# Performance work log

Hardware: AMD Instinct MI355X
Metric: run time of the kernel (lower is better)

## Reference

```python
import jax, jax.numpy as jnp
import numpy as np

K_POS, K_NEG = 3, 2
MIN_D = 9  # min_dist=8 bumped to next odd, as in _nms_topk
BN_EPS = 1e-5


def _conv(x, w, pad):
    return jax.lax.conv_general_dilated(
        x, w, (1, 1), [(pad, pad), (pad, pad)],
        dimension_numbers=('NCHW', 'OIHW', 'NCHW'))


def _bn(x, g, b, m, v):
    scale = g * jax.lax.rsqrt(v + BN_EPS)  # inference-mode BN
    return x * scale[None, :, None, None] + (b - m * scale)[None, :, None, None]


def _head(x, w1, g1, b1, m1, v1, w2, g2, b2, m2, v2, w3, b3, out_hw):
    h = jax.nn.relu(_bn(_conv(x, w1, 1), g1, b1, m1, v1))
    h = jax.nn.relu(_bn(_conv(h, w2, 1), g2, b2, m2, v2))
    logits = _conv(h, w3, 0) + b3[None, :, None, None]
    B = logits.shape[0]
    # F.interpolate(mode='bilinear', align_corners=False) == half-pixel bilinear resize
    logits = jax.image.resize(logits, (B, 1, out_hw, out_hw), method='bilinear')
    return logits


def _sample_one(smap, key):
    # smap: [H, W] sigmoid heatmap for one sample
    H, W = smap.shape
    # --- positive points: NMS-style peak top-k ---
    local_max = jax.lax.reduce_window(
        smap, -jnp.inf, jax.lax.max, (MIN_D, MIN_D), (1, 1), 'SAME')
    is_peak = (smap == local_max) & (smap > 0.1)
    masked = jnp.where(is_peak, smap, -jnp.inf).reshape(-1)
    vals, idx = jax.lax.top_k(masked, K_POS)
    valid = jnp.isfinite(vals)  # slots corresponding to real peaks
    xs = jnp.where(valid, (idx % W).astype(jnp.float32), 0.0)
    ys = jnp.where(valid, (idx // W).astype(jnp.float32), 0.0)
    pos_lab = jnp.where(valid, 1, -1).astype(jnp.int32)
    # fallback: no peak at all -> single argmax point in slot 0
    amax = jnp.argmax(smap)
    any_peak = valid[0]
    xs = xs.at[0].set(jnp.where(any_peak, xs[0], (amax % W).astype(jnp.float32)))
    ys = ys.at[0].set(jnp.where(any_peak, ys[0], (amax // W).astype(jnp.float32)))
    pos_lab = pos_lab.at[0].set(1)  # slot 0 is always a positive point
    pos = jnp.stack([xs, ys], axis=1)  # [K_POS, 2] (x, y)
    # --- negative points: uniform sample from low-response region ---
    low = (smap < 0.3).reshape(-1)
    low_fb = (smap < smap.max()).reshape(-1)
    mask = jnp.where(jnp.any(low), low, low_fb)
    n = mask.sum()
    # stable argsort puts masked-in (True) flat indices first, in index order
    order = jnp.argsort(jnp.logical_not(mask))
    u = jax.random.uniform(key, (K_NEG,))
    ridx = jnp.minimum((u * jnp.maximum(n, 1).astype(jnp.float32)).astype(jnp.int32),
                       jnp.maximum(n - 1, 0))
    sel = order[ridx]
    neg = jnp.stack([sel % W, sel // W], axis=1).astype(jnp.float32)
    neg = jnp.where(n > 0, neg, jnp.zeros_like(neg))
    neg_lab = jnp.zeros((K_NEG,), jnp.int32)
    coords = jnp.concatenate([pos, neg], axis=0)      # [K_POS+K_NEG, 2]
    labels = jnp.concatenate([pos_lab, neg_lab], axis=0)
    return coords, labels


def setup_inputs() -> dict:
    key = jax.random.key(0)
    ks = jax.random.split(key, 4)
    B, C, h, w = 32, 256, 64, 64
    HID = 64
    x = jax.random.normal(ks[0], (B, C, h, w), jnp.float32)
    w1 = jax.random.normal(ks[1], (HID, C, 3, 3), jnp.float32) * 0.03  # kaiming-ish
    w2 = jax.random.normal(ks[2], (HID, HID, 3, 3), jnp.float32) * 0.06
    w3 = jax.random.normal(ks[3], (1, HID, 1, 1), jnp.float32) * 0.17
    b3 = jnp.full((1,), -2.0, jnp.float32)
    ones = jnp.ones((HID,), jnp.float32)
    zeros = jnp.zeros((HID,), jnp.float32)
    return {
        'encoder_features': x,
        'w1': w1, 'g1': ones, 'b1': zeros, 'm1': zeros, 'v1': ones,
        'w2': w2, 'g2': ones, 'b2': zeros, 'm2': zeros, 'v2': ones,
        'w3': w3, 'b3': b3,
        'output_size': 256,
    }


def reference(encoder_features, w1, g1, b1, m1, v1, w2, g2, b2, m2, v2, w3, b3, output_size):
    logits = _head(encoder_features, w1, g1, b1, m1, v1, w2, g2, b2, m2, v2, w3, b3, output_size)
    heatmap = jax.nn.sigmoid(logits)  # [B, 1, H, W]
    B = heatmap.shape[0]
    keys = jax.random.split(jax.random.key(42), B)
    coords, labels = jax.vmap(_sample_one)(heatmap[:, 0], keys)
    point_coords = coords[:, None].astype(jnp.float32)  # [B, 1, K, 2]
    point_labels = labels[:, None].astype(jnp.int32)    # [B, 1, K]
    return heatmap, point_coords, point_labels, logits
```

## Files before the change

### kernel.cpp

```cpp
#include <hip/hip_runtime.h>
#include <stdint.h>
#include <math.h>

#define NEG_INF (-__builtin_inff())
#define IDX_SENT 0x7fffffff

__device__ __forceinline__ void threefry2x32(uint32_t k0, uint32_t k1,
                                             uint32_t x0, uint32_t x1,
                                             uint32_t* o0, uint32_t* o1) {
  const uint32_t ks2 = k0 ^ k1 ^ 0x1BD11BDAu;
  uint32_t ks[3] = {k0, k1, ks2};
  const int rot[2][4] = {{13, 15, 26, 6}, {17, 29, 16, 24}};
  x0 += ks[0];
  x1 += ks[1];
#pragma unroll
  for (int i = 0; i < 5; ++i) {
#pragma unroll
    for (int j = 0; j < 4; ++j) {
      const int r = rot[i & 1][j];
      x0 += x1;
      x1 = (x1 << r) | (x1 >> (32 - r));
      x1 ^= x0;
    }
    x0 += ks[(i + 1) % 3];
    x1 += ks[(i + 2) % 3] + (uint32_t)(i + 1);
  }
  *o0 = x0;
  *o1 = x1;
}

__device__ __forceinline__ float bits_to_uniform(uint32_t bits) {
  return __uint_as_float((bits >> 9) | 0x3f800000u) - 1.0f;
}

__device__ __forceinline__ void top3_insert(float v, int idx, float tv[3], int ti[3]) {
  if ((v > tv[2]) || (v == tv[2] && idx < ti[2])) {
    tv[2] = v; ti[2] = idx;
    if ((tv[2] > tv[1]) || (tv[2] == tv[1] && ti[2] < ti[1])) {
      float fv = tv[1]; int fi = ti[1];
      tv[1] = tv[2]; ti[1] = ti[2];
      tv[2] = fv;     ti[2] = fi;
      if ((tv[1] > tv[0]) || (tv[1] == tv[0] && ti[1] < ti[0])) {
        fv = tv[0]; fi = ti[0];
        tv[0] = tv[1]; ti[0] = ti[1];
        tv[1] = fv;    ti[1] = fi;
      }
    }
  }
}

__global__ __launch_bounds__(256) void transpose_w4(
    const float* __restrict__ w, float* __restrict__ wt, int IC9) {
  const int idx = blockIdx.x * 256 + threadIdx.x;
  const int qrow = idx >> 6;
  const int oc = idx & 63;
  const float4 v = *(const float4*)&w[(size_t)oc * IC9 + qrow * 4];
  wt[(size_t)(qrow * 4 + 0) * 64 + oc] = v.x;
  wt[(size_t)(qrow * 4 + 1) * 64 + oc] = v.y;
  wt[(size_t)(qrow * 4 + 2) * 64 + oc] = v.z;
  wt[(size_t)(qrow * 4 + 3) * 64 + oc] = v.w;
}

template <int IC>
__global__ __launch_bounds__(256, 4) void conv3x3_bn_relu(
    const float* __restrict__ x, const float* __restrict__ wt,
    const float* __restrict__ g, const float* __restrict__ bb,
    const float* __restrict__ m, const float* __restrict__ vv,
    float* __restrict__ out) {
  __shared__ float xs[8][18][20];
  __shared__ float wsh[72][32];

  const int tid = threadIdx.x;
  const int blk = blockIdx.x;
  const int b = blk >> 5;
  const int tile = (blk >> 1) & 15;
  const int och = blk & 1;
  const int by = (tile >> 2) << 4;
  const int bx = (tile & 3) << 4;
  const int ocg = tid & 7;
  const int pg = tid >> 3;
  const int pr = pg >> 1;
  const int pc = (pg & 1) << 3;

  const int sic = tid >> 5;
  const int sc = tid & 31;
  const int gx = bx + sc - 1;
  const bool cok = (sc < 18) && (gx >= 0) && (gx < 64);

  float acc[8][4];
#pragma unroll
  for (int p = 0; p < 8; ++p)
#pragma unroll
    for (int j = 0; j < 4; ++j) acc[p][j] = 0.0f;

  for (int icb = 0; icb < IC; icb += 8) {
    const float* xp = x + ((size_t)b * IC + icb + sic) * 4096;
#pragma unroll
    for (int r = 0; r < 18; ++r) {
      const int gy = by + r - 1;
      float val = 0.0f;
      if (cok && gy >= 0 && gy < 64) val = xp[gy * 64 + gx];
      if (sc < 18) xs[sic][r][sc] = val;
    }
    const float* wp = wt + (size_t)icb * 9 * 64 + (och << 5);
    const int srow0 = tid >> 5;
    const int socl = tid & 31;
#pragma unroll
    for (int q = 0; q < 9; ++q) {
      const int row = (q << 3) + srow0;
      wsh[row][socl] = wp[row * 64 + socl];
    }
    __syncthreads();

    for (int ic = 0; ic < 8; ++ic) {
#pragma unroll
      for (int ky = 0; ky < 3; ++ky) {
        const float* row = &xs[ic][pr + ky][pc];
        float xv[10];
        *(float4*)&xv[0] = *(const float4*)&row[0];
        *(float4*)&xv[4] = *(const float4*)&row[4];
        *(float2*)&xv[8] = *(const float2*)&row[8];
#pragma unroll
        for (int kx = 0; kx < 3; ++kx) {
          const float4 wq = *(const float4*)&wsh[ic * 9 + ky * 3 + kx][ocg << 2];
#pragma unroll
          for (int p = 0; p < 8; ++p) {
            acc[p][0] = fmaf(xv[p + kx], wq.x, acc[p][0]);
            acc[p][1] = fmaf(xv[p + kx], wq.y, acc[p][1]);
            acc[p][2] = fmaf(xv[p + kx], wq.z, acc[p][2]);
            acc[p][3] = fmaf(xv[p + kx], wq.w, acc[p][3]);
          }
        }
      }
    }
    __syncthreads();
  }

#pragma unroll
  for (int j = 0; j < 4; ++j) {
    const int oc = (och << 5) + (ocg << 2) + j;
    const float sc2 = g[oc] * (1.0f / sqrtf(vv[oc] + 1e-5f));
    const float sh = bb[oc] - m[oc] * sc2;
#pragma unroll
    for (int p = 0; p < 8; ++p) {
      float o = fmaf(acc[p][j], sc2, sh);
      o = fmaxf(o, 0.0f);
      out[(((size_t)b * 64 + oc) * 64 + (by + pr)) * 64 + (bx + pc + p)] = o;
    }
  }
}

__global__ __launch_bounds__(256) void logits64_k(
    const float* __restrict__ h2, const float* __restrict__ w3,
    const float* __restrict__ b3, float* __restrict__ lg64) {
  const int blk = blockIdx.x;
  const int b = blk >> 4;
  const int p = ((blk & 15) << 8) + threadIdx.x;
  __shared__ float wv[64];
  if (threadIdx.x < 64) wv[threadIdx.x] = w3[threadIdx.x];
  __syncthreads();
  float s = b3[0];
  const float* hp = h2 + (size_t)b * 64 * 4096 + p;
  for (int oc = 0; oc < 64; ++oc)
    s = fmaf(hp[(size_t)oc * 4096], wv[oc], s);
  lg64[b * 4096 + p] = s;
}

__global__ __launch_bounds__(256) void upsample_k(
    const float* __restrict__ lg64, float* __restrict__ logits,
    float* __restrict__ heat) {
  const int blk = blockIdx.x;
  const int b = blk >> 6;
  const int qq = ((blk & 63) << 10) + (threadIdx.x << 2);
  const float* lg = lg64 + b * 4096;
  const int oy = qq >> 8;
  const float sy = (float)oy * 0.25f - 0.375f;
  const float fy = floorf(sy);
  const int y0 = (int)fy;
  const float ty = sy - fy;
  const int y0c = y0 < 0 ? 0 : y0;
  const int y1c = (y0 + 1) > 63 ? 63 : (y0 + 1);
  const float* r0 = lg + y0c * 64;
  const float* r1 = lg + y1c * 64;
  float4 lo, he;
  float* lop = (float*)&lo;
  float* hep = (float*)&he;
#pragma unroll
  for (int j = 0; j < 4; ++j) {
    const int ox = (qq & 255) + j;
    const float sx = (float)ox * 0.25f - 0.375f;
    const float fx = floorf(sx);
    const int x0 = (int)fx;
    const float tx = sx - fx;
    const int x0c = x0 < 0 ? 0 : x0;
    const int x1c = (x0 + 1) > 63 ? 63 : (x0 + 1);
    const float v00 = r0[x0c], v01 = r0[x1c];
    const float v10 = r1[x0c], v11 = r1[x1c];
    const float vtop = v00 + (v01 - v00) * tx;
    const float vbot = v10 + (v11 - v10) * tx;
    const float val = vtop + (vbot - vtop) * ty;
    lop[j] = val;
    hep[j] = 1.0f / (1.0f + expf(-val));
  }
  const size_t o = (size_t)b * 65536 + qq;
  *(float4*)(logits + o) = lo;
  *(float4*)(heat + o) = he;
}

__global__ __launch_bounds__(256) void pos_stripe(
    const float* __restrict__ heat, float* __restrict__ cand) {
  const int b = blockIdx.x >> 4;
  const int stripe = blockIdx.x & 15;
  const int y0 = stripe << 4;
  const float* s = heat + (size_t)b * 65536;
  const int tid = threadIdx.x;
  __shared__ float sm[24][256];
  __shared__ float rm[24][256];
  __shared__ float rv[256 * 3];
  __shared__ int ri[256 * 3];
  __shared__ float mvv[256];
  __shared__ int mii[256];
  __shared__ float rv2[24];
  __shared__ int ri2[24];
  __shared__ float mv2[8];
  __shared__ int mi2[8];

  for (int l = tid; l < 24 * 256; l += 256) {
    const int rr = l >> 8, xx = l & 255;
    const int gy = y0 - 4 + rr;
    sm[rr][xx] = (gy >= 0 && gy < 256) ? s[gy * 256 + xx] : NEG_INF;
  }
  __syncthreads();
  for (int l = tid; l < 24 * 256; l += 256) {
    const int rr = l >> 8, xx = l & 255;
    const int lo = (xx - 4 < 0) ? 0 : xx - 4;
    const int hi = (xx + 4 > 255) ? 255 : xx + 4;
    float mx = NEG_INF;
    for (int x2 = lo; x2 <= hi; ++x2) mx = fmaxf(mx, sm[rr][x2]);
    rm[rr][xx] = mx;
  }
  __syncthreads();

  float tv[3] = {NEG_INF, NEG_INF, NEG_INF};
  int ti[3] = {IDX_SENT, IDX_SENT, IDX_SENT};
  float bmax = NEG_INF;
  int bidx = IDX_SENT;
  for (int l = tid; l < 16 * 256; l += 256) {
    const int ry = l >> 8, xx = l & 255;
    const int lr = ry + 4;
    const float v = sm[lr][xx];
    float lm = rm[lr - 4][xx];
#pragma unroll
    for (int d = -3; d <= 4; ++d) lm = fmaxf(lm, rm[lr + d][xx]);
    const int gidx = (y0 + ry) * 256 + xx;
    if (v > bmax) { bmax = v; bidx = gidx; }
    if (v == lm && v > 0.1f) top3_insert(v, gidx, tv, ti);
  }

  rv[tid * 3 + 0] = tv[0]; rv[tid * 3 + 1] = tv[1]; rv[tid * 3 + 2] = tv[2];
  ri[tid * 3 + 0] = ti[0]; ri[tid * 3 + 1] = ti[1]; ri[tid * 3 + 2] = ti[2];
  mvv[tid] = bmax; mii[tid] = bidx;
  __syncthreads();

  if (tid < 8) {
    float av[3] = {NEG_INF, NEG_INF, NEG_INF};
    int ai[3] = {IDX_SENT, IDX_SENT, IDX_SENT};
    float am = NEG_INF; int amI = IDX_SENT;
    for (int t = tid * 32; t < tid * 32 + 32; ++t) {
      for (int k = 0; k < 3; ++k) top3_insert(rv[t * 3 + k], ri[t * 3 + k], av, ai);
      if (mvv[t] > am || (mvv[t] == am && mii[t] < amI)) { am = mvv[t]; amI = mii[t]; }
    }
    rv2[tid * 3 + 0] = av[0]; rv2[tid * 3 + 1] = av[1]; rv2[tid * 3 + 2] = av[2];
    ri2[tid * 3 + 0] = ai[0]; ri2[tid * 3 + 1] = ai[1]; ri2[tid * 3 + 2] = ai[2];
    mv2[tid] = am; mi2[tid] = amI;
  }
  __syncthreads();

  if (tid == 0) {
    float fv[3] = {NEG_INF, NEG_INF, NEG_INF};
    int fi[3] = {IDX_SENT, IDX_SENT, IDX_SENT};
    for (int t = 0; t < 24; ++t) top3_insert(rv2[t], ri2[t], fv, fi);
    float gbv = NEG_INF; int gbi = IDX_SENT;
    for (int t = 0; t < 8; ++t)
      if (mv2[t] > gbv || (mv2[t] == gbv && mi2[t] < gbi)) { gbv = mv2[t]; gbi = mi2[t]; }
    float* c = cand + ((size_t)b * 16 + stripe) * 8;
    c[0] = fv[0]; c[1] = __int_as_float(fi[0]);
    c[2] = fv[1]; c[3] = __int_as_float(fi[1]);
    c[4] = fv[2]; c[5] = __int_as_float(fi[2]);
    c[6] = gbv;   c[7] = __int_as_float(gbi);
  }
}

__global__ void pos_final(const float* __restrict__ cand,
                          float* __restrict__ coords, float* __restrict__ labels) {
  const int b = blockIdx.x;
  if (threadIdx.x != 0) return;
  float fv[3] = {NEG_INF, NEG_INF, NEG_INF};
  int fi[3] = {IDX_SENT, IDX_SENT, IDX_SENT};
  float gbv = NEG_INF; int gbi = IDX_SENT;
  for (int st = 0; st < 16; ++st) {
    const float* c = cand + ((size_t)b * 16 + st) * 8;
    for (int k = 0; k < 3; ++k)
      top3_insert(c[2 * k], __float_as_int(c[2 * k + 1]), fv, fi);
    const float mv = c[6]; const int mi = __float_as_int(c[7]);
    if (mv > gbv || (mv == gbv && mi < gbi)) { gbv = mv; gbi = mi; }
  }
  float* co = coords + (size_t)b * 10;
  float* la = labels + (size_t)b * 5;
  const bool any_peak = (fi[0] != IDX_SENT);
  const int i0 = any_peak ? fi[0] : gbi;
  co[0] = (float)(i0 & 255);
  co[1] = (float)(i0 >> 8);
  la[0] = 1.0f;
  for (int k = 1; k < 3; ++k) {
    const bool valid = (fi[k] != IDX_SENT);
    co[k * 2 + 0] = valid ? (float)(fi[k] & 255) : 0.0f;
    co[k * 2 + 1] = valid ? (float)(fi[k] >> 8) : 0.0f;
    la[k] = valid ? 1.0f : -1.0f;
  }
}

__global__ __launch_bounds__(256) void neg_count(
    const float* __restrict__ heat, float* __restrict__ ncnt,
    float* __restrict__ pmax) {
  const int blk = blockIdx.x;
  const int b = blk >> 2;
  const int part = blk & 3;
  const int tid = threadIdx.x;
  const int chunk = (part << 8) + tid;
  const float4* s = (const float4*)(heat + (size_t)b * 65536 + chunk * 64);
  int c = 0;
  float mx = NEG_INF;
  for (int i = 0; i < 16; ++i) {
    const float4 v = s[i];
    c += (v.x < 0.3f) + (v.y < 0.3f) + (v.z < 0.3f) + (v.w < 0.3f);
    mx = fmaxf(mx, fmaxf(fmaxf(v.x, v.y), fmaxf(v.z, v.w)));
  }
  ncnt[b * 1024 + chunk] = (float)c;
  __shared__ float mxs[256];
  mxs[tid] = mx;
  __syncthreads();
  if (tid == 0) {
    float g = NEG_INF;
    for (int t = 0; t < 256; ++t) g = fmaxf(g, mxs[t]);
    pmax[blk] = g;
  }
}

__global__ __launch_bounds__(256) void neg_select(
    const float* __restrict__ heat, const float* __restrict__ ncnt,
    const float* __restrict__ pmax, float* __restrict__ coords,
    float* __restrict__ labels) {
  const int b = blockIdx.x;
  const int tid = threadIdx.x;
  const float* s = heat + (size_t)b * 65536;
  __shared__ float cnt[1024];
  __shared__ float c256[256];
  __shared__ int pfx[257];
  __shared__ float thr_s;
  __shared__ int fb_s;
  __shared__ int n_s;
  __shared__ int ridx_s[2];

  for (int l = tid; l < 1024; l += 256) cnt[l] = ncnt[b * 1024 + l];
  __syncthreads();
  c256[tid] = cnt[4 * tid] + cnt[4 * tid + 1] + cnt[4 * tid + 2] + cnt[4 * tid + 3];
  __syncthreads();
  if (tid == 0) {
    int tot = 0;
    for (int t = 0; t < 256; ++t) tot += (int)c256[t];
    const float gm = fmaxf(fmaxf(pmax[b * 4], pmax[b * 4 + 1]),
                           fmaxf(pmax[b * 4 + 2], pmax[b * 4 + 3]));
    fb_s = (tot > 0) ? 0 : 1;
    thr_s = (tot > 0) ? 0.3f : gm;
  }
  __syncthreads();
  if (fb_s) {
    const float t2 = thr_s;
    const int base = tid * 256;
    int c = 0;
    for (int i = 0; i < 256; ++i) c += (s[base + i] < t2) ? 1 : 0;
    c256[tid] = (float)c;
    __syncthreads();
  }
  if (tid == 0) {
    int run = 0;
    for (int t = 0; t < 256; ++t) { pfx[t] = run; run += (int)c256[t]; }
    pfx[256] = run;
    const int n = run;
    n_s = n;
    uint32_t k0, k1, a0, a1;
    threefry2x32(0u, 42u, 0u, (uint32_t)b, &k0, &k1);
    threefry2x32(k0, k1, 0u, 0u, &a0, &a1);
    const uint32_t bits0 = a0 ^ a1;
    threefry2x32(k0, k1, 0u, 1u, &a0, &a1);
    const uint32_t bits1 = a0 ^ a1;
    const float u0 = bits_to_uniform(bits0);
    const float u1 = bits_to_uniform(bits1);
    const float nf = (float)(n > 1 ? n : 1);
    int r0 = (int)(u0 * nf);
    int r1 = (int)(u1 * nf);
    const int rmax = (n - 1 > 0) ? n - 1 : 0;
    ridx_s[0] = r0 < rmax ? r0 : rmax;
    ridx_s[1] = r1 < rmax ? r1 : rmax;
    labels[(size_t)b * 5 + 3] = 0.0f;
    labels[(size_t)b * 5 + 4] = 0.0f;
    if (n == 0) {
      coords[(size_t)b * 10 + 6] = 0.0f; coords[(size_t)b * 10 + 7] = 0.0f;
      coords[(size_t)b * 10 + 8] = 0.0f; coords[(size_t)b * 10 + 9] = 0.0f;
    }
  }
  __syncthreads();
  const int n = n_s;
  if (n > 0) {
    const float t2 = thr_s;
    const int p0 = pfx[tid], p1 = pfx[tid + 1];
    const int base = tid * 256;
    for (int j = 0; j < 2; ++j) {
      const int r = ridx_s[j];
      if (r >= p0 && r < p1) {
        int need = r - p0;
        int sel = -1;
        for (int i = 0; i < 256; ++i) {
          if (s[base + i] < t2) {
            if (need == 0) { sel = base + i; break; }
            --need;
          }
        }
        coords[(size_t)b * 10 + 6 + j * 2 + 0] = (float)(sel & 255);
        coords[(size_t)b * 10 + 6 + j * 2 + 1] = (float)(sel >> 8);
      }
    }
  }
}

extern "C" void kernel_launch(void* const* d_in, const int* in_sizes, int n_in,
                              void* d_out, int out_size, void* d_ws, size_t ws_size,
                              hipStream_t stream) {
  (void)in_sizes; (void)n_in; (void)out_size; (void)ws_size;
  const float* x  = (const float*)d_in[0];
  const float* w1 = (const float*)d_in[1];
  const float* g1 = (const float*)d_in[2];
  const float* b1 = (const float*)d_in[3];
  const float* m1 = (const float*)d_in[4];
  const float* v1 = (const float*)d_in[5];
  const float* w2 = (const float*)d_in[6];
  const float* g2 = (const float*)d_in[7];
  const float* b2 = (const float*)d_in[8];
  const float* m2 = (const float*)d_in[9];
  const float* v2 = (const float*)d_in[10];
  const float* w3 = (const float*)d_in[11];
  const float* b3 = (const float*)d_in[12];

  float* out = (float*)d_out;
  float* heat = out;
  float* coords = out + (size_t)32 * 65536;
  float* labels = coords + 320;
  float* logits = labels + 160;

  float* w1t = logits;
  float* w2t = logits + 147456;

  float* h1 = (float*)d_ws;
  float* h2 = h1 + (size_t)32 * 64 * 64 * 64;
  float* lg64 = h1;
  float* cand = h1 + 131072;
  float* ncnt = h1 + 135168;
  float* pmax = h1 + 167936;

  transpose_w4<<<144, 256, 0, stream>>>(w1, w1t, 2304);
  transpose_w4<<<36, 256, 0, stream>>>(w2, w2t, 576);
  conv3x3_bn_relu<256><<<1024, 256, 0, stream>>>(x, w1t, g1, b1, m1, v1, h1);
  conv3x3_bn_relu<64><<<1024, 256, 0, stream>>>(h1, w2t, g2, b2, m2, v2, h2);
  logits64_k<<<512, 256, 0, stream>>>(h2, w3, b3, lg64);
  upsample_k<<<2048, 256, 0, stream>>>(lg64, logits, heat);
  pos_stripe<<<512, 256, 0, stream>>>(heat, cand);
  pos_final<<<32, 64, 0, stream>>>(cand, coords, labels);
  neg_count<<<128, 256, 0, stream>>>(heat, ncnt, pmax);
  neg_select<<<32, 256, 0, stream>>>(heat, ncnt, pmax, coords, labels);
}
```

Before: 917.6 us.

## Widen conv blocks to all 64 output channels with two output rows per thread

New measurement: 952.4 us. 1.04x slower.

```diff
diff --git a/kernel.cpp b/kernel.cpp
--- a/kernel.cpp
+++ b/kernel.cpp
@@ -62,36 +62,40 @@
 }
 
 template <int IC>
-__global__ __launch_bounds__(256, 4) void conv3x3_bn_relu(
+__global__ __launch_bounds__(256, 2) void conv3x3_bn_relu(
     const float* __restrict__ x, const float* __restrict__ wt,
     const float* __restrict__ g, const float* __restrict__ bb,
     const float* __restrict__ m, const float* __restrict__ vv,
     float* __restrict__ out) {
   __shared__ float xs[8][18][20];
-  __shared__ float wsh[72][32];
+  __shared__ float wsh[72][64];
 
   const int tid = threadIdx.x;
-  const int blk = blockIdx.x;
-  const int b = blk >> 5;
-  const int tile = (blk >> 1) & 15;
-  const int och = blk & 1;
+  const int b = blockIdx.x >> 4;
+  const int tile = blockIdx.x & 15;
   const int by = (tile >> 2) << 4;
   const int bx = (tile & 3) << 4;
-  const int ocg = tid & 7;
-  const int pg = tid >> 3;
-  const int pr = pg >> 1;
-  const int pc = (pg & 1) << 3;
+  const int ocg = tid & 15;
+  const int pg = tid >> 4;
+  const int rg = pg >> 1;
+  const int cg = pg & 1;
+  const int pc = cg << 3;
+  const int pr = rg << 1;
 
   const int sic = tid >> 5;
   const int sc = tid & 31;
   const int gx = bx + sc - 1;
   const bool cok = (sc < 18) && (gx >= 0) && (gx < 64);
-
-  float acc[8][4];
-#pragma unroll
-  for (int p = 0; p < 8; ++p)
-#pragma unroll
-    for (int j = 0; j < 4; ++j) acc[p][j] = 0.0f;
+  const int swr = tid >> 6;
+  const int soc = tid & 63;
+
+  float acc[2][8][4];
+#pragma unroll
+  for (int o = 0; o < 2; ++o)
+#pragma unroll
+    for (int p = 0; p < 8; ++p)
+#pragma unroll
+      for (int j = 0; j < 4; ++j) acc[o][p][j] = 0.0f;
 
   for (int icb = 0; icb < IC; icb += 8) {
     const float* xp = x + ((size_t)b * IC + icb + sic) * 4096;
@@ -102,33 +106,41 @@
       if (cok && gy >= 0 && gy < 64) val = xp[gy * 64 + gx];
       if (sc < 18) xs[sic][r][sc] = val;
     }
-    const float* wp = wt + (size_t)icb * 9 * 64 + (och << 5);
-    const int srow0 = tid >> 5;
-    const int socl = tid & 31;
-#pragma unroll
-    for (int q = 0; q < 9; ++q) {
-      const int row = (q << 3) + srow0;
-      wsh[row][socl] = wp[row * 64 + socl];
+    const float* wp = wt + (size_t)icb * 9 * 64;
+#pragma unroll
+    for (int q = 0; q < 18; ++q) {
+      const int row = (q << 2) + swr;
+      wsh[row][soc] = wp[row * 64 + soc];
     }
     __syncthreads();
 
     for (int ic = 0; ic < 8; ++ic) {
-#pragma unroll
-      for (int ky = 0; ky < 3; ++ky) {
-        const float* row = &xs[ic][pr + ky][pc];
+      float4 wq[9];
+#pragma unroll
+      for (int k = 0; k < 9; ++k)
+        wq[k] = *(const float4*)&wsh[ic * 9 + k][ocg << 2];
+
+#pragma unroll
+      for (int i = 0; i < 4; ++i) {
+        const float* row = &xs[ic][pr + i][pc];
         float xv[10];
         *(float4*)&xv[0] = *(const float4*)&row[0];
         *(float4*)&xv[4] = *(const float4*)&row[4];
         *(float2*)&xv[8] = *(const float2*)&row[8];
 #pragma unroll
-        for (int kx = 0; kx < 3; ++kx) {
-          const float4 wq = *(const float4*)&wsh[ic * 9 + ky * 3 + kx][ocg << 2];
-#pragma unroll
-          for (int p = 0; p < 8; ++p) {
-            acc[p][0] = fmaf(xv[p + kx], wq.x, acc[p][0]);
-            acc[p][1] = fmaf(xv[p + kx], wq.y, acc[p][1]);
-            acc[p][2] = fmaf(xv[p + kx], wq.z, acc[p][2]);
-            acc[p][3] = fmaf(xv[p + kx], wq.w, acc[p][3]);
+        for (int o = 0; o < 2; ++o) {
+          const int ky = i - o;
+          if (ky < 0 || ky > 2) continue;
+#pragma unroll
+          for (int kx = 0; kx < 3; ++kx) {
+            const float4 w4 = wq[ky * 3 + kx];
+#pragma unroll
+            for (int p = 0; p < 8; ++p) {
+              acc[o][p][0] = fmaf(xv[p + kx], w4.x, acc[o][p][0]);
+              acc[o][p][1] = fmaf(xv[p + kx], w4.y, acc[o][p][1]);
+              acc[o][p][2] = fmaf(xv[p + kx], w4.z, acc[o][p][2]);
+              acc[o][p][3] = fmaf(xv[p + kx], w4.w, acc[o][p][3]);
+            }
           }
         }
       }
@@ -138,14 +150,23 @@
 
 #pragma unroll
   for (int j = 0; j < 4; ++j) {
-    const int oc = (och << 5) + (ocg << 2) + j;
+    const int oc = (ocg << 2) + j;
     const float sc2 = g[oc] * (1.0f / sqrtf(vv[oc] + 1e-5f));
     const float sh = bb[oc] - m[oc] * sc2;
 #pragma unroll
-    for (int p = 0; p < 8; ++p) {
-      float o = fmaf(acc[p][j], sc2, sh);
-      o = fmaxf(o, 0.0f);
-      out[(((size_t)b * 64 + oc) * 64 + (by + pr)) * 64 + (bx + pc + p)] = o;
+    for (int o = 0; o < 2; ++o) {
+      float4 v0, v1;
+      v0.x = fmaxf(fmaf(acc[o][0][j], sc2, sh), 0.0f);
+      v0.y = fmaxf(fmaf(acc[o][1][j], sc2, sh), 0.0f);
+      v0.z = fmaxf(fmaf(acc[o][2][j], sc2, sh), 0.0f);
+      v0.w = fmaxf(fmaf(acc[o][3][j], sc2, sh), 0.0f);
+      v1.x = fmaxf(fmaf(acc[o][4][j], sc2, sh), 0.0f);
+      v1.y = fmaxf(fmaf(acc[o][5][j], sc2, sh), 0.0f);
+      v1.z = fmaxf(fmaf(acc[o][6][j], sc2, sh), 0.0f);
+      v1.w = fmaxf(fmaf(acc[o][7][j], sc2, sh), 0.0f);
+      float* op = &out[(((size_t)b * 64 + oc) * 64 + (by + pr + o)) * 64 + bx + pc];
+      *(float4*)&op[0] = v0;
+      *(float4*)&op[4] = v1;
     }
   }
 }
@@ -470,8 +491,8 @@
 
   transpose_w4<<<144, 256, 0, stream>>>(w1, w1t, 2304);
   transpose_w4<<<36, 256, 0, stream>>>(w2, w2t, 576);
-  conv3x3_bn_relu<256><<<1024, 256, 0, stream>>>(x, w1t, g1, b1, m1, v1, h1);
-  conv3x3_bn_relu<64><<<1024, 256, 0, stream>>>(h1, w2t, g2, b2, m2, v2, h2);
+  conv3x3_bn_relu<256><<<512, 256, 0, stream>>>(x, w1t, g1, b1, m1, v1, h1);
+  conv3x3_bn_relu<64><<<512, 256, 0, stream>>>(h1, w2t, g2, b2, m2, v2, h2);
   logits64_k<<<512, 256, 0, stream>>>(h2, w3, b3, lg64);
   upsample_k<<<2048, 256, 0, stream>>>(lg64, logits, heat);
   pos_stripe<<<512, 256, 0, stream>>>(heat, cand);
```
